# Optimization experiments

Measured on AMD Instinct MI355X. Metric: run time of the kernel, lower is better.

The kernel has to match this reference:

```python
import jax, jax.numpy as jnp
import numpy as np
import math

B, S, D_MODEL = 2, 2048, 1024
H = 16
DK = D_MODEL // H          # 64, down-proj per-stream dim
NOPE, ROPE = 128, 64
D_HEAD = NOPE + ROPE       # 192 = d_latent // H
D_LATENT = H * D_HEAD      # 3072
ROT_DIM = 2 * ((ROPE // 2) // 2)  # rotary dim actually rotated = qk_rope_dim//2 = 32
EPS = 1e-6


def _rmsnorm(x, w):
    out = x * jax.lax.rsqrt(jnp.mean(x * x, axis=-1, keepdims=True) + EPS)
    return out * w


def _apply_rope(x):
    # x: [b, h, s, d]; rotate first ROT_DIM channels, interleaved pairing
    s = x.shape[-2]
    inv_freq = 1.0 / (10000.0 ** (jnp.arange(0, ROT_DIM, 2, dtype=jnp.float32) / ROT_DIM))
    freqs = jnp.arange(s, dtype=jnp.float32)[:, None] * inv_freq[None, :]  # [s, ROT_DIM//2]
    freqs = jnp.repeat(freqs, 2, axis=-1)  # [s, ROT_DIM], (f0,f0,f1,f1,...)
    cos, sin = jnp.cos(freqs), jnp.sin(freqs)
    xl, xr = x[..., :ROT_DIM], x[..., ROT_DIM:]
    x1, x2 = xl[..., 0::2], xl[..., 1::2]
    rot = jnp.stack([-x2, x1], axis=-1).reshape(xl.shape)
    xl = xl * cos + rot * sin
    return jnp.concatenate([xl, xr], axis=-1)


def setup_inputs() -> dict:
    key = jax.random.key(0)
    ks = jax.random.split(key, 5)
    sc = 0.02
    x = jax.random.normal(ks[0], (B, S, D_MODEL), jnp.float32)
    mask = jnp.broadcast_to(jnp.tril(jnp.ones((S, S), jnp.int32)), (B, S, S))
    w_down = jax.random.normal(ks[1], (D_MODEL, 3 * DK), jnp.float32) * sc
    rms_w = jnp.ones((3 * DK,), jnp.float32)
    w_up = jax.random.normal(ks[2], (3 * DK, 3 * D_LATENT), jnp.float32) * sc
    w_o = jax.random.normal(ks[3], (D_LATENT, D_MODEL), jnp.float32) * sc
    return {"x": x, "mask": mask, "w_down": w_down, "rms_w": rms_w, "w_up": w_up, "w_o": w_o}


def reference(x, mask, w_down, rms_w, w_up, w_o):
    h = x @ w_down                        # [b, s, 3*dk]
    h = _rmsnorm(h, rms_w)
    qkv = h @ w_up                        # [b, s, 3*d_latent]
    q, k, v = jnp.split(qkv, 3, axis=-1)  # each [b, s, d_latent]

    def to_heads(t):
        # einops '(d h)': d outer, h inner
        return t.reshape(B, S, D_HEAD, H).transpose(0, 3, 1, 2)  # [b, h, s, d]

    q, k, v = to_heads(q), to_heads(k), to_heads(v)
    q_nope, q_rope = q[..., :NOPE], q[..., NOPE:]
    k_nope, k_rope = k[..., :NOPE], k[..., NOPE:]
    q_rope = _apply_rope(q_rope)
    k_rope = _apply_rope(k_rope)

    scores = (jnp.einsum('bhid,bhjd->bhij', q_nope, k_nope)
              + jnp.einsum('bhid,bhjd->bhij', q_rope, k_rope))
    scores = scores / math.sqrt(NOPE + ROPE)
    scores = jnp.where(mask[:, None] == 0, -1e9, scores)
    attn = jax.nn.softmax(scores, axis=-1)

    out = jnp.einsum('bhij,bhjd->bhid', attn, v)        # [b, h, s, d]
    out = out.transpose(0, 2, 1, 3).reshape(B, S, D_LATENT)  # 'b h s d -> b s (h d)'
    return out @ w_o
```

## Files before the change

### kernel.cpp

```cpp
#include <hip/hip_runtime.h>
#include <stdint.h>
#include <stddef.h>


typedef __bf16 bf16x8 __attribute__((ext_vector_type(8)));
typedef float  f32x4  __attribute__((ext_vector_type(4)));

#define MFMA16x16(a,b,c) __builtin_amdgcn_mfma_f32_16x16x32_bf16((a),(b),(c),0,0,0)

__device__ __forceinline__ uint16_t f2bf(float f){
  union { float f; uint32_t u; } v; v.f = f;
  uint32_t u = v.u + 0x7fffu + ((v.u >> 16) & 1u);
  return (uint16_t)(u >> 16);
}
__device__ __forceinline__ bf16x8 load_frag(const uint16_t* p){
  uint4 u = *reinterpret_cast<const uint4*>(p);
  return __builtin_bit_cast(bf16x8, u);
}
__device__ __forceinline__ f32x4 fzero(){
  f32x4 z = {0.f, 0.f, 0.f, 0.f};
  return z;
}
__device__ __forceinline__ uint32_t pack2(float a, float b){
  return (uint32_t)f2bf(a) | ((uint32_t)f2bf(b) << 16);
}
__device__ __forceinline__ void gl2lds16(const uint16_t* g, uint16_t* l){
  __builtin_amdgcn_global_load_lds(
      (const __attribute__((address_space(1))) uint32_t*)g,
      (__attribute__((address_space(3))) uint32_t*)l,
      16, 0, 0);
}

__global__ __launch_bounds__(256) void k_transpose_cvt(const float* __restrict__ in,
                                                       uint16_t* __restrict__ out,
                                                       int R, int C){
  __shared__ float t[32][33];
  const int tc = blockIdx.x * 32;
  const int tr = blockIdx.y * 32;
  const int j = threadIdx.x & 31, i0 = threadIdx.x >> 5;
  for(int ii = 0; ii < 4; ++ii){
    int r = i0 + ii * 8;
    t[r][j] = in[(size_t)(tr + r) * C + tc + j];
  }
  __syncthreads();
  for(int ii = 0; ii < 4; ++ii){
    int c = i0 + ii * 8;
    out[(size_t)(tc + c) * R + tr + j] = f2bf(t[j][c]);
  }
}

__global__ __launch_bounds__(256) void k_down_mfma(const float* __restrict__ x,
                                                   const uint16_t* __restrict__ wdt,
                                                   const float* __restrict__ rms_w,
                                                   uint16_t* __restrict__ h_out){
  __shared__ __align__(16) uint16_t as[32 * 64];
  __shared__ float hsq[32];
  const int tid  = threadIdx.x;
  const int wave = tid >> 6, lane = tid & 63;
  const int ml = lane & 15, qd = lane >> 4;
  const int m0 = blockIdx.x * 32;
  const int n0w = wave * 48;
  if(tid < 32) hsq[tid] = 0.f;

  f32x4 acc[2][3];
#pragma unroll
  for(int mt = 0; mt < 2; ++mt)
#pragma unroll
    for(int nt = 0; nt < 3; ++nt) acc[mt][nt] = fzero();

  const int srow = tid >> 3, sc = tid & 7;
  for(int kt = 0; kt < 16; ++kt){
    const float* src = x + (size_t)(m0 + srow) * 1024 + kt * 64 + sc * 8;
    float4 a = *reinterpret_cast<const float4*>(src);
    float4 b = *reinterpret_cast<const float4*>(src + 4);
    uint4 pk;
    pk.x = pack2(a.x, a.y); pk.y = pack2(a.z, a.w);
    pk.z = pack2(b.x, b.y); pk.w = pack2(b.z, b.w);
    __syncthreads();
    *reinterpret_cast<uint4*>(as + srow * 64 + ((sc ^ (srow & 7)) * 8)) = pk;
    __syncthreads();
#pragma unroll
    for(int kk = 0; kk < 2; ++kk){
      bf16x8 af[2];
#pragma unroll
      for(int mt = 0; mt < 2; ++mt){
        int row = mt * 16 + ml;
        af[mt] = load_frag(as + row * 64 + (((kk * 4 + qd) ^ (row & 7)) * 8));
      }
#pragma unroll
      for(int nt = 0; nt < 3; ++nt){
        bf16x8 bfr = load_frag(wdt + (size_t)(n0w + nt * 16 + ml) * 1024 + kt * 64 + kk * 32 + qd * 8);
#pragma unroll
        for(int mt = 0; mt < 2; ++mt)
          acc[mt][nt] = MFMA16x16(af[mt], bfr, acc[mt][nt]);
      }
    }
  }
  __syncthreads();
#pragma unroll
  for(int mt = 0; mt < 2; ++mt)
#pragma unroll
    for(int r = 0; r < 4; ++r){
      float s = acc[mt][0][r]*acc[mt][0][r] + acc[mt][1][r]*acc[mt][1][r] + acc[mt][2][r]*acc[mt][2][r];
#pragma unroll
      for(int off = 1; off < 16; off <<= 1) s += __shfl_xor(s, off);
      if(ml == 0) atomicAdd(&hsq[mt * 16 + qd * 4 + r], s);
    }
  __syncthreads();
  float rw[3];
#pragma unroll
  for(int nt = 0; nt < 3; ++nt) rw[nt] = rms_w[n0w + nt * 16 + ml];
#pragma unroll
  for(int mt = 0; mt < 2; ++mt)
#pragma unroll
    for(int r = 0; r < 4; ++r){
      int row = mt * 16 + qd * 4 + r;
      float scl = rsqrtf(hsq[row] * (1.0f / 192.0f) + 1e-6f);
#pragma unroll
      for(int nt = 0; nt < 3; ++nt)
        h_out[(size_t)(m0 + row) * 192 + n0w + nt * 16 + ml] = f2bf(acc[mt][nt][r] * scl * rw[nt]);
    }
}

__global__ __launch_bounds__(256) void k_gemm_up(const uint16_t* __restrict__ hmat,
                                                 const uint16_t* __restrict__ wt,
                                                 uint16_t* __restrict__ q_t,
                                                 uint16_t* __restrict__ k_t,
                                                 uint16_t* __restrict__ v_t){
  __shared__ __align__(16) uint16_t rp[16 * 129 * 8];
  const int wave = threadIdx.x >> 6, lane = threadIdx.x & 63;
  const int ml = lane & 15, qd = lane >> 4;
  const int m0 = blockIdx.y * 32;
  const int bx = blockIdx.x;
  const int which = bx / 6;
  const int d0b = (bx % 6) * 32;
  const int n0w = bx * 512 + wave * 128;
  const int d0w = d0b + wave * 8;

  bf16x8 af[2][6];
#pragma unroll
  for(int mt = 0; mt < 2; ++mt)
#pragma unroll
    for(int kk = 0; kk < 6; ++kk)
      af[mt][kk] = load_frag(hmat + (size_t)(m0 + mt * 16 + ml) * 192 + kk * 32 + qd * 8);

  f32x4 acc[8][2];
#pragma unroll
  for(int nt = 0; nt < 8; ++nt){ acc[nt][0] = fzero(); acc[nt][1] = fzero(); }
#pragma unroll
  for(int nt = 0; nt < 8; ++nt){
#pragma unroll
    for(int kk = 0; kk < 6; ++kk){
      bf16x8 b = load_frag(wt + (size_t)(n0w + nt * 16 + ml) * 192 + kk * 32 + qd * 8);
      acc[nt][0] = MFMA16x16(af[0][kk], b, acc[nt][0]);
      acc[nt][1] = MFMA16x16(af[1][kk], b, acc[nt][1]);
    }
  }

  const int b   = m0 >> 11;
  const int s0  = m0 & 2047;
  const int kt2 = s0 >> 6;
  const int row0 = s0 & 63;
  uint4* rp4 = (uint4*)rp;

  if(which < 2){
    const float qs = which ? 1.0f : 0.07216878364870322f;
    const bool rope = (d0w >= 128) && (d0w < 160);
#pragma unroll
    for(int mt = 0; mt < 2; ++mt)
#pragma unroll
      for(int r = 0; r < 4; ++r){
        int t = mt * 16 + qd * 4 + r;
        int s = s0 + t;
        float v[8];
#pragma unroll
        for(int nt = 0; nt < 8; ++nt) v[nt] = acc[nt][mt][r] * qs;
        if(rope){
#pragma unroll
          for(int pi = 0; pi < 4; ++pi){
            int fi = (d0w + 2 * pi - 128) >> 1;
            float invf = __expf(-(float)fi * 0.5756462732485114f);
            float sn, cs;
            sincosf((float)s * invf, &sn, &cs);
            float e = v[2 * pi], o = v[2 * pi + 1];
            v[2 * pi]     = e * cs - o * sn;
            v[2 * pi + 1] = o * cs + e * sn;
          }
        }
        uint4 pk;
        pk.x = pack2(v[0], v[1]); pk.y = pack2(v[2], v[3]);
        pk.z = pack2(v[4], v[5]); pk.w = pack2(v[6], v[7]);
        rp4[ml * 129 + t * 4 + (wave ^ (t & 3))] = pk;
      }
  } else {
#pragma unroll
    for(int nt = 0; nt < 8; ++nt){
      int dl = wave * 8 + nt;
#pragma unroll
      for(int mt = 0; mt < 2; ++mt){
        int jc = mt * 2 + (qd >> 1);
        int slot = ml * 129 + dl * 4 + (jc ^ (dl & 3));
        uint2 pk;
        pk.x = pack2(acc[nt][mt][0], acc[nt][mt][1]);
        pk.y = pack2(acc[nt][mt][2], acc[nt][mt][3]);
        *(reinterpret_cast<uint2*>(rp + slot * 8) + (qd & 1)) = pk;
      }
    }
  }
  __syncthreads();

  if(which < 2){
    uint16_t* dst = which ? k_t : q_t;
    const int cb = d0b >> 3;
#pragma unroll
    for(int it = 0; it < 8; ++it){
      int h = wave * 4 + (it & 3), rhalf = it >> 2;
      int tloc = rhalf * 16 + (lane >> 2), p = lane & 3;
      int row = row0 + tloc;
      uint4 val = rp4[h * 129 + tloc * 4 + p];
      size_t off = ((size_t)(b * 16 + h) * 32 + kt2) * 12288
                 + (size_t)row * 192 + ((cb ^ (tloc & 4)) + p) * 8;
      *reinterpret_cast<uint4*>(dst + off) = val;
    }
  } else {
    const int cs0 = row0 >> 3;
#pragma unroll
    for(int it = 0; it < 8; ++it){
      int h = wave * 4 + (it & 3), dhalf = it >> 2;
      int dl = dhalf * 16 + (lane >> 2), p = lane & 3;
      uint4 val = rp4[h * 129 + dl * 4 + p];
      size_t off = ((size_t)(b * 16 + h) * 32 + kt2) * 12288
                 + (size_t)(d0b + dl) * 64 + ((cs0 ^ (dl & 4)) + p) * 8;
      *reinterpret_cast<uint4*>(v_t + off) = val;
    }
  }
}

__global__ __launch_bounds__(256, 3) void k_attn(const uint16_t* __restrict__ q_t,
                                                 const uint16_t* __restrict__ k_t,
                                                 const uint16_t* __restrict__ v_t,
                                                 uint16_t* __restrict__ attn_out){
  __shared__ __align__(16) uint16_t ks[64 * 192];
  __shared__ __align__(16) uint16_t vs[208 * 64];
  const int tid  = threadIdx.x;
  const int wave = tid >> 6;
  const int lane = tid & 63;
  const int ml   = lane & 15;
  const int qd   = lane >> 4;
  const int L    = blockIdx.x;
  const int idx  = L >> 3;
  const int qt   = 31 - (idx & 31);
  const int bh   = (L & 7) + ((idx >> 5) << 3);

  {
    uint32_t* vw = (uint32_t*)vs;
    vw[6144 + tid] = 0x3F803F80u;
    vw[6400 + tid] = 0x3F803F80u;
  }

  {
    const uint16_t* qtile = q_t + ((size_t)bh * 32 + qt) * (64 * 192);
#pragma unroll
    for(int it = 0; it < 6; ++it){
      int seg = it * 4 + wave;
      gl2lds16(qtile + seg * 512 + lane * 8, ks + seg * 512);
    }
  }
  __syncthreads();
  bf16x8 qf[6];
  {
    int row = wave * 16 + ml;
#pragma unroll
    for(int kk = 0; kk < 6; ++kk)
      qf[kk] = load_frag(ks + row * 192 + (((kk * 4 + qd) ^ (row & 7)) * 8));
  }

  f32x4 o[13];
#pragma unroll
  for(int i = 0; i < 13; ++i) o[i] = fzero();

  for(int kt = 0; kt <= qt; ++kt){
    __syncthreads();
    const uint16_t* ktile = k_t + ((size_t)bh * 32 + kt) * (64 * 192);
    const uint16_t* vtile = v_t + ((size_t)bh * 32 + kt) * (192 * 64);
#pragma unroll
    for(int it = 0; it < 6; ++it){
      int seg = it * 4 + wave;
      gl2lds16(ktile + seg * 512 + lane * 8, ks + seg * 512);
    }
#pragma unroll
    for(int it = 0; it < 6; ++it){
      int seg = it * 4 + wave;
      gl2lds16(vtile + seg * 512 + lane * 8, vs + seg * 512);
    }
    __syncthreads();

    float p[4][4];
    const bool diag = (kt == qt);
#pragma unroll
    for(int nt = 0; nt < 4; ++nt){
      f32x4 a = fzero();
      int row = nt * 16 + ml;
#pragma unroll
      for(int kk = 0; kk < 6; ++kk){
        bf16x8 b = load_frag(ks + row * 192 + (((kk * 4 + qd) ^ (row & 7)) * 8));
        a = MFMA16x16(qf[kk], b, a);
      }
#pragma unroll
      for(int r = 0; r < 4; ++r){
        float v = a[r];
        if(diag){
          int i = qt * 64 + wave * 16 + qd * 4 + r;
          int j = kt * 64 + nt * 16 + ml;
          if(j > i) v = -1e9f;
        }
        p[nt][r] = __expf(v);
      }
    }

    __syncthreads();
    uint16_t* psw = ks + wave * 1024;
#pragma unroll
    for(int nt = 0; nt < 4; ++nt)
#pragma unroll
      for(int r = 0; r < 4; ++r){
        int rp2 = qd * 4 + r;
        int col = nt * 16 + ml;
        int c = (col >> 3) ^ (rp2 & 7);
        psw[rp2 * 64 + c * 8 + (col & 7)] = f2bf(p[nt][r]);
      }
#pragma unroll
    for(int kk2 = 0; kk2 < 2; ++kk2){
      int cp = (kk2 * 4 + qd) ^ (ml & 7);
      bf16x8 pa = load_frag(psw + ml * 64 + cp * 8);
#pragma unroll
      for(int dt = 0; dt < 13; ++dt){
        int row = dt * 16 + ml;
        int cv = (kk2 * 4 + qd) ^ (row & 7);
        bf16x8 vb = load_frag(vs + row * 64 + cv * 8);
        o[dt] = MFMA16x16(pa, vb, o[dt]);
      }
    }
  }

  const int hh = bh & 15, b = bh >> 4;
#pragma unroll
  for(int r = 0; r < 4; ++r){
    int i = qt * 64 + wave * 16 + qd * 4 + r;
    float inv = 1.0f / o[12][r];
    size_t obase = ((size_t)b * 2048 + i) * 3072 + hh * 192;
#pragma unroll
    for(int dt = 0; dt < 12; ++dt)
      attn_out[obase + dt * 16 + ml] = f2bf(o[dt][r] * inv);
  }
}

__global__ __launch_bounds__(256) void k_gemm_o_tile(const uint16_t* __restrict__ a,
                                                     const uint16_t* __restrict__ wt,
                                                     float* __restrict__ part){
  __shared__ __align__(16) uint16_t as[128 * 64];
  __shared__ __align__(16) uint16_t bs[128 * 64];
  const int wave = threadIdx.x >> 6, lane = threadIdx.x & 63;
  const int ml = lane & 15, qd = lane >> 4;
  const int m0 = blockIdx.y * 128, n0 = blockIdx.x * 128;
  const int kz = blockIdx.z;
  const int mo = (wave >> 1) * 64, no = (wave & 1) * 64;

  const int lrow = lane >> 3;
  const int gch  = (lane & 7) ^ (lrow & 7);
  const uint16_t* abase = a  + (size_t)(m0 + lrow) * 3072 + kz * 1536 + gch * 8;
  const uint16_t* bbase = wt + (size_t)(n0 + lrow) * 3072 + kz * 1536 + gch * 8;

  f32x4 acc[4][4];
#pragma unroll
  for(int mt = 0; mt < 4; ++mt)
#pragma unroll
    for(int nt = 0; nt < 4; ++nt) acc[mt][nt] = fzero();

  for(int kt = 0; kt < 24; ++kt){
    __syncthreads();
#pragma unroll
    for(int it = 0; it < 4; ++it){
      int seg = it * 4 + wave;
      gl2lds16(abase + (size_t)seg * 24576 + kt * 64, as + seg * 512);
      gl2lds16(bbase + (size_t)seg * 24576 + kt * 64, bs + seg * 512);
    }
    __syncthreads();
#pragma unroll
    for(int ks2 = 0; ks2 < 2; ++ks2){
      bf16x8 af[4], bfr[4];
#pragma unroll
      for(int mt = 0; mt < 4; ++mt){
        int row = mo + mt * 16 + ml;
        af[mt] = load_frag(as + row * 64 + (((ks2 * 4 + qd) ^ (row & 7)) * 8));
      }
#pragma unroll
      for(int nt = 0; nt < 4; ++nt){
        int row = no + nt * 16 + ml;
        bfr[nt] = load_frag(bs + row * 64 + (((ks2 * 4 + qd) ^ (row & 7)) * 8));
      }
#pragma unroll
      for(int mt = 0; mt < 4; ++mt)
#pragma unroll
        for(int nt = 0; nt < 4; ++nt)
          acc[mt][nt] = MFMA16x16(af[mt], bfr[nt], acc[mt][nt]);
    }
  }

  float* dst = part + (size_t)kz * 4096 * 1024;
#pragma unroll
  for(int mt = 0; mt < 4; ++mt)
#pragma unroll
    for(int nt = 0; nt < 4; ++nt)
#pragma unroll
      for(int r = 0; r < 4; ++r){
        int row = m0 + mo + mt * 16 + qd * 4 + r;
        int col = n0 + no + nt * 16 + ml;
        dst[(size_t)row * 1024 + col] = acc[mt][nt][r];
      }
}

__global__ __launch_bounds__(256) void k_addout(const float* __restrict__ part,
                                                float* __restrict__ out){
  int i = blockIdx.x * 256 + threadIdx.x;
  const float4* p0 = (const float4*)part;
  const float4* p1 = p0 + (size_t)1048576;
  float4 a = p0[i], b = p1[i];
  float4 c; c.x = a.x + b.x; c.y = a.y + b.y; c.z = a.z + b.z; c.w = a.w + b.w;
  ((float4*)out)[i] = c;
}


extern "C" void kernel_launch(void* const* d_in, const int* in_sizes, int n_in,
                              void* d_out, int out_size, void* d_ws, size_t ws_size,
                              hipStream_t stream) {
  (void)in_sizes; (void)n_in; (void)out_size; (void)ws_size;
  const float* x      = (const float*)d_in[0];
  const float* w_down = (const float*)d_in[2];
  const float* rms_w  = (const float*)d_in[3];
  const float* w_up   = (const float*)d_in[4];
  const float* w_o    = (const float*)d_in[5];
  float* out = (float*)d_out;

  char* ws = (char*)d_ws;
  uint16_t* h_bf   = (uint16_t*)(ws);
  uint16_t* w_up_t = (uint16_t*)(ws + 1572864);
  uint16_t* w_o_t  = (uint16_t*)(ws + 5111808);
  uint16_t* w_dn_t = (uint16_t*)(ws + 11403264);
  uint16_t* q_tb   = (uint16_t*)(ws + 11796480);
  uint16_t* k_tb   = (uint16_t*)(ws + 36962304);
  uint16_t* v_tb   = (uint16_t*)(ws + 62128128);
  uint16_t* attnO  = (uint16_t*)(ws + 87293952);
  float*    part   = (float*)(ws + 11796480);

  k_transpose_cvt<<<dim3(288, 6), 256, 0, stream>>>(w_up, w_up_t, 192, 9216);
  k_transpose_cvt<<<dim3(32, 96), 256, 0, stream>>>(w_o,  w_o_t,  3072, 1024);
  k_transpose_cvt<<<dim3(6, 32),  256, 0, stream>>>(w_down, w_dn_t, 1024, 192);
  k_down_mfma<<<128, 256, 0, stream>>>(x, w_dn_t, rms_w, h_bf);
  k_gemm_up<<<dim3(18, 128), 256, 0, stream>>>(h_bf, w_up_t, q_tb, k_tb, v_tb);
  k_attn<<<1024, 256, 0, stream>>>(q_tb, k_tb, v_tb, attnO);
  k_gemm_o_tile<<<dim3(8, 32, 2), 256, 0, stream>>>(attnO, w_o_t, part);
  k_addout<<<4096, 256, 0, stream>>>(part, out);
}
```

Baseline: 354.4 us.

## Double attention query tile to 128 rows and merge weight transposes into one launch

The attention kernel now handles 128 query rows per block, two 16-row groups per wave, so each K/V tile loaded into LDS is reused across twice as many queries. The launch count halves, masking becomes a zeroed exponent on the diagonal tiles, and waves skip the fully masked last tile. P gets its own LDS region, which removes one barrier per iteration. In exchange, register pressure rises (two accumulator sets of 13 fragments), occupancy drops to 2 blocks per SM, and there are fewer blocks to balance the causal workload. The three weight transpose launches are also merged into a single kernel.

```diff
diff --git a/kernel.cpp b/kernel.cpp
--- a/kernel.cpp
+++ b/kernel.cpp
@@ -31,12 +31,19 @@
       16, 0, 0);
 }
 
-__global__ __launch_bounds__(256) void k_transpose_cvt(const float* __restrict__ in,
-                                                       uint16_t* __restrict__ out,
-                                                       int R, int C){
+__global__ __launch_bounds__(256) void k_transpose_all(const float* __restrict__ w_up,
+                                                       const float* __restrict__ w_o,
+                                                       const float* __restrict__ w_down,
+                                                       uint16_t* __restrict__ w_up_t,
+                                                       uint16_t* __restrict__ w_o_t,
+                                                       uint16_t* __restrict__ w_dn_t){
   __shared__ float t[32][33];
-  const int tc = blockIdx.x * 32;
-  const int tr = blockIdx.y * 32;
+  int id = blockIdx.x;
+  const float* in; uint16_t* out; int R, C, bx, by;
+  if(id < 1728){ in = w_up;  out = w_up_t; R = 192;  C = 9216; bx = id % 288; by = id / 288; }
+  else if(id < 4800){ id -= 1728; in = w_o; out = w_o_t; R = 3072; C = 1024; bx = id % 32; by = id / 32; }
+  else { id -= 4800; in = w_down; out = w_dn_t; R = 1024; C = 192; bx = id % 6; by = id / 6; }
+  const int tc = bx * 32, tr = by * 32;
   const int j = threadIdx.x & 31, i0 = threadIdx.x >> 5;
   for(int ii = 0; ii < 4; ++ii){
     int r = i0 + ii * 8;
@@ -236,12 +243,14 @@
   }
 }
 
-__global__ __launch_bounds__(256, 3) void k_attn(const uint16_t* __restrict__ q_t,
+__global__ __launch_bounds__(256, 2) void k_attn(const uint16_t* __restrict__ q_t,
                                                  const uint16_t* __restrict__ k_t,
                                                  const uint16_t* __restrict__ v_t,
                                                  uint16_t* __restrict__ attn_out){
-  __shared__ __align__(16) uint16_t ks[64 * 192];
-  __shared__ __align__(16) uint16_t vs[208 * 64];
+  __shared__ __align__(16) uint16_t lds[33792];
+  uint16_t* ks = lds;
+  uint16_t* vs = lds + 12288;
+  uint16_t* ps = lds + 25600;
   const int tid  = threadIdx.x;
   const int wave = tid >> 6;
   const int lane = tid & 63;
@@ -249,110 +258,119 @@
   const int qd   = lane >> 4;
   const int L    = blockIdx.x;
   const int idx  = L >> 3;
-  const int qt   = 31 - (idx & 31);
-  const int bh   = (L & 7) + ((idx >> 5) << 3);
+  const int qt2  = 15 - (idx & 15);
+  const int bh   = (L & 7) + ((idx >> 4) << 3);
+  const int q0   = qt2 * 128;
+  const int last = 2 * qt2 + 1;
 
   {
-    uint32_t* vw = (uint32_t*)vs;
-    vw[6144 + tid] = 0x3F803F80u;
-    vw[6400 + tid] = 0x3F803F80u;
-  }
-
+    uint32_t* vw = (uint32_t*)(lds + 24576);
+    vw[tid] = 0x3F803F80u;
+    vw[tid + 256] = 0x3F803F80u;
+  }
   {
-    const uint16_t* qtile = q_t + ((size_t)bh * 32 + qt) * (64 * 192);
-#pragma unroll
-    for(int it = 0; it < 6; ++it){
+    const uint16_t* qsrc = q_t + ((size_t)bh * 32 + 2 * qt2) * 12288;
+#pragma unroll
+    for(int it = 0; it < 12; ++it){
       int seg = it * 4 + wave;
-      gl2lds16(qtile + seg * 512 + lane * 8, ks + seg * 512);
+      gl2lds16(qsrc + seg * 512 + lane * 8, lds + seg * 512);
     }
   }
   __syncthreads();
-  bf16x8 qf[6];
-  {
-    int row = wave * 16 + ml;
+  bf16x8 qf[2][6];
+#pragma unroll
+  for(int mg = 0; mg < 2; ++mg){
+    int row = wave * 32 + mg * 16 + ml;
+    int t64 = row >> 6, rl = row & 63;
 #pragma unroll
     for(int kk = 0; kk < 6; ++kk)
-      qf[kk] = load_frag(ks + row * 192 + (((kk * 4 + qd) ^ (row & 7)) * 8));
-  }
-
-  f32x4 o[13];
-#pragma unroll
-  for(int i = 0; i < 13; ++i) o[i] = fzero();
-
-  for(int kt = 0; kt <= qt; ++kt){
-    __syncthreads();
-    const uint16_t* ktile = k_t + ((size_t)bh * 32 + kt) * (64 * 192);
-    const uint16_t* vtile = v_t + ((size_t)bh * 32 + kt) * (192 * 64);
+      qf[mg][kk] = load_frag(lds + t64 * 12288 + rl * 192 + (((kk * 4 + qd) ^ (rl & 7)) * 8));
+  }
+
+  f32x4 o[2][13];
+#pragma unroll
+  for(int mg = 0; mg < 2; ++mg)
+#pragma unroll
+    for(int i = 0; i < 13; ++i) o[mg][i] = fzero();
+
+  for(int kt = 0; kt <= last; ++kt){
+    __syncthreads();
+    const uint16_t* ktile = k_t + ((size_t)bh * 32 + kt) * 12288;
+    const uint16_t* vtile = v_t + ((size_t)bh * 32 + kt) * 12288;
 #pragma unroll
     for(int it = 0; it < 6; ++it){
       int seg = it * 4 + wave;
       gl2lds16(ktile + seg * 512 + lane * 8, ks + seg * 512);
-    }
-#pragma unroll
-    for(int it = 0; it < 6; ++it){
-      int seg = it * 4 + wave;
       gl2lds16(vtile + seg * 512 + lane * 8, vs + seg * 512);
     }
     __syncthreads();
 
-    float p[4][4];
-    const bool diag = (kt == qt);
-#pragma unroll
-    for(int nt = 0; nt < 4; ++nt){
-      f32x4 a = fzero();
-      int row = nt * 16 + ml;
-#pragma unroll
-      for(int kk = 0; kk < 6; ++kk){
-        bf16x8 b = load_frag(ks + row * 192 + (((kk * 4 + qd) ^ (row & 7)) * 8));
-        a = MFMA16x16(qf[kk], b, a);
-      }
-#pragma unroll
-      for(int r = 0; r < 4; ++r){
-        float v = a[r];
-        if(diag){
-          int i = qt * 64 + wave * 16 + qd * 4 + r;
-          int j = kt * 64 + nt * 16 + ml;
-          if(j > i) v = -1e9f;
+    const bool full_skip = (kt == last) && (wave < 2);
+    if(!full_skip){
+      const bool need_mask = (wave < 2) ? (kt == last - 1) : (kt == last);
+#pragma unroll
+      for(int mg = 0; mg < 2; ++mg){
+        float p[4][4];
+#pragma unroll
+        for(int nt = 0; nt < 4; ++nt){
+          f32x4 a = fzero();
+          int row = nt * 16 + ml;
+#pragma unroll
+          for(int kk = 0; kk < 6; ++kk){
+            bf16x8 bfr = load_frag(ks + row * 192 + (((kk * 4 + qd) ^ (row & 7)) * 8));
+            a = MFMA16x16(qf[mg][kk], bfr, a);
+          }
+#pragma unroll
+          for(int r = 0; r < 4; ++r){
+            float e = __expf(a[r]);
+            if(need_mask){
+              int i = q0 + wave * 32 + mg * 16 + qd * 4 + r;
+              int j = kt * 64 + nt * 16 + ml;
+              if(j > i) e = 0.f;
+            }
+            p[nt][r] = e;
+          }
         }
-        p[nt][r] = __expf(v);
-      }
-    }
-
-    __syncthreads();
-    uint16_t* psw = ks + wave * 1024;
-#pragma unroll
-    for(int nt = 0; nt < 4; ++nt)
-#pragma unroll
-      for(int r = 0; r < 4; ++r){
-        int rp2 = qd * 4 + r;
-        int col = nt * 16 + ml;
-        int c = (col >> 3) ^ (rp2 & 7);
-        psw[rp2 * 64 + c * 8 + (col & 7)] = f2bf(p[nt][r]);
-      }
-#pragma unroll
-    for(int kk2 = 0; kk2 < 2; ++kk2){
-      int cp = (kk2 * 4 + qd) ^ (ml & 7);
-      bf16x8 pa = load_frag(psw + ml * 64 + cp * 8);
-#pragma unroll
-      for(int dt = 0; dt < 13; ++dt){
-        int row = dt * 16 + ml;
-        int cv = (kk2 * 4 + qd) ^ (row & 7);
-        bf16x8 vb = load_frag(vs + row * 64 + cv * 8);
-        o[dt] = MFMA16x16(pa, vb, o[dt]);
+        uint16_t* psw = ps + wave * 2048 + mg * 1024;
+#pragma unroll
+        for(int nt = 0; nt < 4; ++nt)
+#pragma unroll
+          for(int r = 0; r < 4; ++r){
+            int rp2 = qd * 4 + r;
+            int col = nt * 16 + ml;
+            int c = (col >> 3) ^ (rp2 & 7);
+            psw[rp2 * 64 + c * 8 + (col & 7)] = f2bf(p[nt][r]);
+          }
+      }
+#pragma unroll
+      for(int kk2 = 0; kk2 < 2; ++kk2){
+        int cp = (kk2 * 4 + qd) ^ (ml & 7);
+        bf16x8 pa0 = load_frag(ps + wave * 2048 + ml * 64 + cp * 8);
+        bf16x8 pa1 = load_frag(ps + wave * 2048 + 1024 + ml * 64 + cp * 8);
+#pragma unroll
+        for(int dt = 0; dt < 13; ++dt){
+          int row = dt * 16 + ml;
+          int cv = (kk2 * 4 + qd) ^ (row & 7);
+          bf16x8 vb = load_frag(vs + row * 64 + cv * 8);
+          o[0][dt] = MFMA16x16(pa0, vb, o[0][dt]);
+          o[1][dt] = MFMA16x16(pa1, vb, o[1][dt]);
+        }
       }
     }
   }
 
   const int hh = bh & 15, b = bh >> 4;
 #pragma unroll
-  for(int r = 0; r < 4; ++r){
-    int i = qt * 64 + wave * 16 + qd * 4 + r;
-    float inv = 1.0f / o[12][r];
-    size_t obase = ((size_t)b * 2048 + i) * 3072 + hh * 192;
-#pragma unroll
-    for(int dt = 0; dt < 12; ++dt)
-      attn_out[obase + dt * 16 + ml] = f2bf(o[dt][r] * inv);
-  }
+  for(int mg = 0; mg < 2; ++mg)
+#pragma unroll
+    for(int r = 0; r < 4; ++r){
+      int i = q0 + wave * 32 + mg * 16 + qd * 4 + r;
+      float inv = 1.0f / o[mg][12][r];
+      size_t obase = ((size_t)b * 2048 + i) * 3072 + hh * 192;
+#pragma unroll
+      for(int dt = 0; dt < 12; ++dt)
+        attn_out[obase + dt * 16 + ml] = f2bf(o[mg][dt][r] * inv);
+    }
 }
 
 __global__ __launch_bounds__(256) void k_gemm_o_tile(const uint16_t* __restrict__ a,
@@ -453,12 +471,10 @@
   uint16_t* attnO  = (uint16_t*)(ws + 87293952);
   float*    part   = (float*)(ws + 11796480);
 
-  k_transpose_cvt<<<dim3(288, 6), 256, 0, stream>>>(w_up, w_up_t, 192, 9216);
-  k_transpose_cvt<<<dim3(32, 96), 256, 0, stream>>>(w_o,  w_o_t,  3072, 1024);
-  k_transpose_cvt<<<dim3(6, 32),  256, 0, stream>>>(w_down, w_dn_t, 1024, 192);
+  k_transpose_all<<<4992, 256, 0, stream>>>(w_up, w_o, w_down, w_up_t, w_o_t, w_dn_t);
   k_down_mfma<<<128, 256, 0, stream>>>(x, w_dn_t, rms_w, h_bf);
   k_gemm_up<<<dim3(18, 128), 256, 0, stream>>>(h_bf, w_up_t, q_tb, k_tb, v_tb);
-  k_attn<<<1024, 256, 0, stream>>>(q_tb, k_tb, v_tb, attnO);
+  k_attn<<<512, 256, 0, stream>>>(q_tb, k_tb, v_tb, attnO);
   k_gemm_o_tile<<<dim3(8, 32, 2), 256, 0, stream>>>(attnO, w_o_t, part);
   k_addout<<<4096, 256, 0, stream>>>(part, out);
 }
```

Result: slower. 379.8 us (+7.2%).
